# Performance work log

Measured on AMD Instinct MI355X. Metric: run time of the kernel, lower is better.

## Reference

```python
import jax, jax.numpy as jnp
import numpy as np

EPS = 1e-6      # vector-neuron epsilon
BN_EPS = 1e-5   # torch BatchNorm eps
NEG = 0.2       # LeakyReLU negative slope
K = 20


def knn_idx(flat, k):
    # flat: [B, D, N] flattened (C*3) features; returns kNN indices [B, N, k]
    xx = jnp.sum(flat * flat, axis=1)                     # [B, N]
    inner = jnp.einsum('bdn,bdm->bnm', flat, flat)        # [B, N, N]
    neg_dist = 2.0 * inner - xx[:, :, None] - xx[:, None, :]
    return jax.lax.top_k(neg_dist, k)[1]                  # [B, N, k]


def graph_feature(x, k):
    # x: [B, C, 3, N] -> [B, 2C, 3, N, k] = cat(neighbor - center, center)
    B, C, _, N = x.shape
    idx = knn_idx(x.reshape(B, C * 3, N), k)              # [B, N, k]
    xt = jnp.transpose(x, (0, 3, 1, 2))                   # [B, N, C, 3]
    nbr = jax.vmap(lambda f, i: f[i])(xt, idx)            # [B, N, k, C, 3]
    ctr = jnp.broadcast_to(xt[:, :, None], nbr.shape)
    feat = jnp.concatenate([nbr - ctr, ctr], axis=3)      # [B, N, k, 2C, 3]
    return jnp.transpose(feat, (0, 3, 4, 1, 2))


def vn_bn(x, w, b):
    # VNBatchNorm (training-mode batch stats): normalize the per-vector norm.
    # x: [B, C, 3, ...]
    norm = jnp.sqrt(jnp.sum(x * x, axis=2)) + EPS         # [B, C, ...]
    axes = (0,) + tuple(range(2, norm.ndim))
    mean = jnp.mean(norm, axis=axes, keepdims=True)
    var = jnp.mean((norm - mean) ** 2, axis=axes, keepdims=True)
    shp = (1, -1) + (1,) * (norm.ndim - 2)
    nbn = (norm - mean) / jnp.sqrt(var + BN_EPS) * w.reshape(shp) + b.reshape(shp)
    return x * jnp.expand_dims(nbn / norm, 2)


def vn_lrelu(x, wf, wd, bnw, bnb):
    # VNLinearLeakyReLU: linear over channel dim, VN batchnorm, directional LeakyReLU
    p = jnp.einsum('oi,bi...->bo...', wf, x)
    p = vn_bn(p, bnw, bnb)
    d = jnp.einsum('oi,bi...->bo...', wd, x)
    dot = jnp.sum(p * d, axis=2, keepdims=True)
    dsq = jnp.sum(d * d, axis=2, keepdims=True)
    mask = (dot >= 0).astype(x.dtype)
    return NEG * p + (1.0 - NEG) * (mask * p + (1.0 - mask) * (p - (dot / (dsq + EPS)) * d))


def setup_inputs() -> dict:
    key = jax.random.key(0)
    ks = jax.random.split(key, 12)
    H, C = 64, 128
    lin = lambda k, o, i: jax.random.normal(k, (o, i), jnp.float32) / np.sqrt(i)
    return {
        'x': jax.random.normal(ks[0], (8, 1024, 3), jnp.float32),
        'w1f': lin(ks[1], H, 2), 'w1d': lin(ks[2], H, 2),
        'bn1w': jnp.ones(H), 'bn1b': jnp.zeros(H),
        'w2f': lin(ks[3], H, 2 * H), 'w2d': lin(ks[4], H, 2 * H),
        'bn2w': jnp.ones(H), 'bn2b': jnp.zeros(H),
        'w3f': lin(ks[5], H, 2 * H), 'w3d': lin(ks[6], H, 2 * H),
        'bn3w': jnp.ones(H), 'bn3b': jnp.zeros(H),
        'w4f': lin(ks[7], H, 2 * H), 'w4d': lin(ks[8], H, 2 * H),
        'bn4w': jnp.ones(H), 'bn4b': jnp.zeros(H),
        'wcf': lin(ks[9], C, 4 * H), 'wcd': lin(ks[10], 1, 4 * H),
        'bncw': jnp.ones(C), 'bncb': jnp.zeros(C),
    }


def reference(x, w1f, w1d, bn1w, bn1b, w2f, w2d, bn2w, bn2b,
              w3f, w3d, bn3w, bn3b, w4f, w4d, bn4w, bn4b,
              wcf, wcd, bncw, bncb):
    pts = jnp.transpose(x, (0, 2, 1))[:, None]            # [B, 1, 3, N]
    h = vn_lrelu(graph_feature(pts, K), w1f, w1d, bn1w, bn1b)
    x1 = jnp.mean(h, axis=-1)                             # [B, H, 3, N]
    h = vn_lrelu(graph_feature(x1, K), w2f, w2d, bn2w, bn2b)
    x2 = jnp.mean(h, axis=-1)
    h = vn_lrelu(graph_feature(x2, K), w3f, w3d, bn3w, bn3b)
    x3 = jnp.mean(h, axis=-1)
    h = vn_lrelu(graph_feature(x3, K), w4f, w4d, bn4w, bn4b)
    x4 = jnp.mean(h, axis=-1)
    cat = jnp.concatenate([x1, x2, x3, x4], axis=1)       # [B, 4H, 3, N]
    out = vn_lrelu(cat, wcf, wcd, bncw, bncb)             # [B, c_dim, 3, N]
    return jnp.mean(out, axis=-1)                         # [B, c_dim, 3]
```

## Files before the change

kernel.cpp:

```cpp
#include <hip/hip_runtime.h>

#define NPTS 1024
#define NB 8
#define KNN 20
#define N3 (3*NPTS)
#define CHT 256
#define BSX (CHT*N3)

constexpr int OFF_X0    = 0;
constexpr int OFF_XFEAT = OFF_X0 + NB*N3;
constexpr int OFF_YAP   = OFF_XFEAT + NB*CHT*N3;
constexpr int OFF_YBP   = OFF_YAP + NB*N3*64;
constexpr int OFF_YAD   = OFF_YBP + NB*N3*64;
constexpr int OFF_YBD   = OFF_YAD + NB*N3*64;
constexpr int OFF_WCFT  = OFF_YBD + NB*N3*64;
constexpr int OFF_STATS = OFF_WCFT + 256*128;
constexpr int OFF_IDX   = OFF_STATS + 5*256;
constexpr int OFF_W4    = OFF_IDX + NB*NPTS*KNN;
constexpr int OFF_PF    = OFF_YAP;
constexpr int OFF_DF    = OFF_YAD;

__global__ __launch_bounds__(256) void k_prep(
    const float* __restrict__ x,
    const float* __restrict__ w1f, const float* __restrict__ w1d,
    const float* __restrict__ w2f, const float* __restrict__ w2d,
    const float* __restrict__ w3f, const float* __restrict__ w3d,
    const float* __restrict__ w4f, const float* __restrict__ w4d,
    const float* __restrict__ wcf,
    float* __restrict__ x0, float* __restrict__ w4, float* __restrict__ wT) {
  int blk = blockIdx.x, tid = threadIdx.x;
  if (blk < 32) {
    int t = blk*256 + tid;
    int b = t >> 10, n = t & 1023;
    const float* p = x + t*3;
    x0[b*N3 + n]          = p[0];
    x0[b*N3 + NPTS + n]   = p[1];
    x0[b*N3 + 2*NPTS + n] = p[2];
  } else if (blk == 32) {
    if (tid < 64) {
      int o = tid;
      float a0 = w1f[o*2], a1 = w1f[o*2+1];
      float d0 = w1d[o*2], d1 = w1d[o*2+1];
      float* dst = w4 + o*4;
      dst[0] = a0; dst[1] = a1 - a0; dst[2] = d0; dst[3] = d1 - d0;
    }
  } else if (blk < 36) {
    int L = blk - 32;
    const float* wf = (L == 1) ? w2f : (L == 2) ? w3f : w4f;
    const float* wd = (L == 1) ? w2d : (L == 2) ? w3d : w4d;
    float* dst = w4 + L*16384;
    for (int u = 0; u < 64; ++u) {
      int e = tid + u*256;
      int i = e >> 8, oc = e & 255, o = oc >> 2, c = oc & 3;
      float v;
      if (c == 0)      v = wf[o*128 + i];
      else if (c == 1) v = wf[o*128 + 64 + i] - wf[o*128 + i];
      else if (c == 2) v = wd[o*128 + i];
      else             v = wd[o*128 + 64 + i] - wd[o*128 + i];
      dst[e] = v;
    }
  } else {
    int e0 = (blk - 36) * 8192;
    for (int u = 0; u < 32; ++u) {
      int e = e0 + tid + u*256;
      int o = e >> 8, i = e & 255;
      wT[i*128 + o] = wcf[e];
    }
  }
}

__global__ __launch_bounds__(512) void k_knn3(const float* __restrict__ Fb, int bs, int D,
                                              int* __restrict__ idxo) {
  __shared__ float xs[2][8][NPTS];
  int g  = blockIdx.x;
  int wg = (g & 7)*32 + (g >> 3);
  int b  = wg >> 5;
  int n0 = (wg & 31) << 5;
  int tid = threadIdx.x;
  int w = tid >> 6, lane = tid & 63;
  int rowbase = n0 + (w << 2);
  const float* f = Fb + (size_t)b*bs;

  float acc[4][16], xxm[16], xxr[4];
  #pragma unroll
  for (int r = 0; r < 4; ++r) xxr[r] = 0.f;
  #pragma unroll
  for (int s = 0; s < 16; ++s) {
    xxm[s] = 0.f;
    #pragma unroll
    for (int r = 0; r < 4; ++r) acc[r][s] = 0.f;
  }

  int cnt0 = (D < 8) ? D : 8;
  #pragma unroll
  for (int u = 0; u < 4; ++u) {
    int e = tid + (u << 9);
    int dd = e >> 8, mq = (e & 255) << 2;
    if (dd < cnt0)
      *(float4*)&xs[0][dd][mq] = *(const float4*)&f[(size_t)dd*NPTS + mq];
  }
  __syncthreads();

  int nt = (D + 7) >> 3;
  for (int t = 0; t < nt; ++t) {
    int cur = t & 1;
    int cnt = D - (t << 3); if (cnt > 8) cnt = 8;
    float4 pf[4];
    if (t + 1 < nt) {
      int d0 = (t + 1) << 3;
      #pragma unroll
      for (int u = 0; u < 4; ++u) {
        int e = tid + (u << 9);
        int dd = e >> 8, mq = (e & 255) << 2;
        pf[u] = *(const float4*)&f[(size_t)(d0 + dd)*NPTS + mq];
      }
    }
    if (cnt == 8) {
      #pragma unroll
      for (int dd = 0; dd < 8; ++dd) {
        float4 rf = *(const float4*)&xs[cur][dd][rowbase];
        xxr[0] = fmaf(rf.x, rf.x, xxr[0]);
        xxr[1] = fmaf(rf.y, rf.y, xxr[1]);
        xxr[2] = fmaf(rf.z, rf.z, xxr[2]);
        xxr[3] = fmaf(rf.w, rf.w, xxr[3]);
        #pragma unroll
        for (int s2 = 0; s2 < 4; ++s2) {
          float4 xm = *(const float4*)&xs[cur][dd][(lane << 2) + (s2 << 8)];
          float xm4[4] = {xm.x, xm.y, xm.z, xm.w};
          #pragma unroll
          for (int q = 0; q < 4; ++q) {
            int s = s2*4 + q;
            xxm[s] = fmaf(xm4[q], xm4[q], xxm[s]);
            acc[0][s] = fmaf(rf.x, xm4[q], acc[0][s]);
            acc[1][s] = fmaf(rf.y, xm4[q], acc[1][s]);
            acc[2][s] = fmaf(rf.z, xm4[q], acc[2][s]);
            acc[3][s] = fmaf(rf.w, xm4[q], acc[3][s]);
          }
        }
      }
    } else {
      for (int dd = 0; dd < cnt; ++dd) {
        float4 rf = *(const float4*)&xs[cur][dd][rowbase];
        xxr[0] = fmaf(rf.x, rf.x, xxr[0]);
        xxr[1] = fmaf(rf.y, rf.y, xxr[1]);
        xxr[2] = fmaf(rf.z, rf.z, xxr[2]);
        xxr[3] = fmaf(rf.w, rf.w, xxr[3]);
        #pragma unroll
        for (int s2 = 0; s2 < 4; ++s2) {
          float4 xm = *(const float4*)&xs[cur][dd][(lane << 2) + (s2 << 8)];
          float xm4[4] = {xm.x, xm.y, xm.z, xm.w};
          #pragma unroll
          for (int q = 0; q < 4; ++q) {
            int s = s2*4 + q;
            xxm[s] = fmaf(xm4[q], xm4[q], xxm[s]);
            acc[0][s] = fmaf(rf.x, xm4[q], acc[0][s]);
            acc[1][s] = fmaf(rf.y, xm4[q], acc[1][s]);
            acc[2][s] = fmaf(rf.z, xm4[q], acc[2][s]);
            acc[3][s] = fmaf(rf.w, xm4[q], acc[3][s]);
          }
        }
      }
    }
    if (t + 1 < nt) {
      int nb = cur ^ 1;
      #pragma unroll
      for (int u = 0; u < 4; ++u) {
        int e = tid + (u << 9);
        int dd = e >> 8, mq = (e & 255) << 2;
        *(float4*)&xs[nb][dd][mq] = pf[u];
      }
    }
    __syncthreads();
  }

  #pragma unroll
  for (int r = 0; r < 4; ++r)
    #pragma unroll
    for (int s = 0; s < 16; ++s)
      acc[r][s] = (2.f*acc[r][s] - xxr[r]) - xxm[s];

  const float NEGINF = -3.402823466e38f;
  #pragma unroll
  for (int pr = 0; pr < 2; ++pr) {
    const int rA = pr*2, rB = pr*2 + 1;
    unsigned clA = 0xFFFFu, clB = 0xFFFFu;
    int winA = 0, winB = 0;
    for (int it = 0; it < KNN; ++it) {
      float boA = NEGINF, boB = NEGINF;
      unsigned bcA = 0u, bcB = 0u;
      #pragma unroll
      for (int s = 0; s < 16; ++s) {
        const unsigned Cs = (unsigned)(((s >> 2) << 8) | (s & 3));
        float vA = acc[rA][s]; vA = (clA == Cs) ? NEGINF : vA; acc[rA][s] = vA;
        if (vA > boA) { boA = vA; bcA = Cs; }
        float vB = acc[rB][s]; vB = (clB == Cs) ? NEGINF : vB; acc[rB][s] = vB;
        if (vB > boB) { boB = vB; bcB = Cs; }
      }
      int mA = (lane << 2) | (int)(bcA & 3u) | (int)(bcA & 0x300u);
      int mB = (lane << 2) | (int)(bcB & 3u) | (int)(bcB & 0x300u);
      float wmA = boA, wmB = boB;
      #pragma unroll
      for (int off = 1; off < 64; off <<= 1) {
        float tA = __shfl_xor(wmA, off, 64);
        float tB = __shfl_xor(wmB, off, 64);
        wmA = fmaxf(wmA, tA);
        wmB = fmaxf(wmB, tB);
      }
      unsigned long long balA = __ballot(boA == wmA);
      int win_mA;
      if (__popcll(balA) == 1) {
        int wl = __ffsll((long long)balA) - 1;
        win_mA = __shfl(mA, wl, 64);
      } else {
        int cA = (boA == wmA) ? (1023 - mA) : -1;
        #pragma unroll
        for (int off = 1; off < 64; off <<= 1) { int tc = __shfl_xor(cA, off, 64); cA = max(cA, tc); }
        win_mA = 1023 - cA;
      }
      clA = (boA == wmA && mA == win_mA) ? bcA : 0xFFFFu;
      if (lane == it) winA = win_mA;
      unsigned long long balB = __ballot(boB == wmB);
      int win_mB;
      if (__popcll(balB) == 1) {
        int wl = __ffsll((long long)balB) - 1;
        win_mB = __shfl(mB, wl, 64);
      } else {
        int cB = (boB == wmB) ? (1023 - mB) : -1;
        #pragma unroll
        for (int off = 1; off < 64; off <<= 1) { int tc = __shfl_xor(cB, off, 64); cB = max(cB, tc); }
        win_mB = 1023 - cB;
      }
      clB = (boB == wmB && mB == win_mB) ? bcB : 0xFFFFu;
      if (lane == it) winB = win_mB;
    }
    if (lane < KNN) {
      idxo[(b*NPTS + rowbase + rA)*KNN + lane] = winA;
      idxo[(b*NPTS + rowbase + rB)*KNN + lane] = winB;
    }
  }
}

__global__ __launch_bounds__(256) void k_linear4(const float* __restrict__ xin, int bsx,
                                                 const float* __restrict__ w4, int DIN,
                                                 float* __restrict__ yAp, float* __restrict__ yBp,
                                                 float* __restrict__ yAd, float* __restrict__ yBd) {
  int tid = threadIdx.x;
  int o = tid & 63, ns = tid >> 6;
  int b = blockIdx.y / 3, v = blockIdx.y % 3;
  int n0 = blockIdx.x * 32 + ns * 8;
  const float* xb = xin + (size_t)b*bsx + v*NPTS + n0;
  float aF[8], bF[8], aD[8], bD[8];
  #pragma unroll
  for (int j = 0; j < 8; ++j) { aF[j] = 0.f; bF[j] = 0.f; aD[j] = 0.f; bD[j] = 0.f; }
  #pragma unroll 4
  for (int i = 0; i < DIN; ++i) {
    float4 wv  = *(const float4*)&w4[(i << 8) + (o << 2)];
    float4 xlo = *(const float4*)&xb[i*N3];
    float4 xhi = *(const float4*)&xb[i*N3 + 4];
    float xv[8] = {xlo.x, xlo.y, xlo.z, xlo.w, xhi.x, xhi.y, xhi.z, xhi.w};
    #pragma unroll
    for (int j = 0; j < 8; ++j) {
      aF[j] = fmaf(wv.x, xv[j], aF[j]);
      bF[j] = fmaf(wv.y, xv[j], bF[j]);
      aD[j] = fmaf(wv.z, xv[j], aD[j]);
      bD[j] = fmaf(wv.w, xv[j], bD[j]);
    }
  }
  int base = ((b*3 + v)*NPTS + n0)*64 + o;
  #pragma unroll
  for (int j = 0; j < 8; ++j) {
    yAp[base + j*64] = aF[j];
    yBp[base + j*64] = bF[j];
    yAd[base + j*64] = aD[j];
    yBd[base + j*64] = bD[j];
  }
}

__global__ __launch_bounds__(256) void k_stats2(const float* __restrict__ yAp, const float* __restrict__ yBp,
                                                const int* __restrict__ idxo, float* __restrict__ statsL) {
  __shared__ float rs[256], rss[256];
  int tid = threadIdx.x; int o = tid & 63, w = tid >> 6;
  int blk = blockIdx.x;
  int wg = ((blk & 7) << 8) | (blk >> 3);
  int b = wg >> 8;
  int n = ((wg & 255) << 2) + w;
  const int* ir = idxo + (b*NPTS + n)*KNN;
  int4 ir0 = *(const int4*)&ir[0],  ir1 = *(const int4*)&ir[4];
  int4 ir2 = *(const int4*)&ir[8],  ir3 = *(const int4*)&ir[12];
  int4 ir4 = *(const int4*)&ir[16];
  int mm[20] = {ir0.x,ir0.y,ir0.z,ir0.w, ir1.x,ir1.y,ir1.z,ir1.w,
                ir2.x,ir2.y,ir2.z,ir2.w, ir3.x,ir3.y,ir3.z,ir3.w,
                ir4.x,ir4.y,ir4.z,ir4.w};
  int i0 = (b*3*NPTS + n)*64 + o;
  float c0 = yBp[i0], c1 = yBp[i0 + NPTS*64], c2 = yBp[i0 + 2*NPTS*64];
  float s = 0.f, ss = 0.f;
  #pragma unroll
  for (int kk = 0; kk < KNN; ++kk) {
    int m = mm[kk];
    int gg = (b*3*NPTS + m)*64 + o;
    float p0 = yAp[gg] + c0;
    float p1 = yAp[gg + NPTS*64] + c1;
    float p2 = yAp[gg + 2*NPTS*64] + c2;
    float nrm = sqrtf(p0*p0 + p1*p1 + p2*p2) + 1e-6f;
    s += nrm; ss = fmaf(nrm, nrm, ss);
  }
  rs[tid] = s; rss[tid] = ss;
  __syncthreads();
  if (tid < 64) {
    float a  = rs[tid]  + rs[tid+64]  + rs[tid+128]  + rs[tid+192];
    float as = rss[tid] + rss[tid+64] + rss[tid+128] + rss[tid+192];
    atomicAdd(&statsL[tid], a);
    atomicAdd(&statsL[128 + tid], as);
  }
}

__global__ __launch_bounds__(256) void k_apply(const float* __restrict__ yAp, const float* __restrict__ yBp,
                                               const float* __restrict__ yAd, const float* __restrict__ yBd,
                                               const int* __restrict__ idxo, const float* __restrict__ statsL,
                                               const float* __restrict__ bnw, const float* __restrict__ bnb,
                                               float* __restrict__ xfeat, int coff) {
  int tid = threadIdx.x; int o = tid & 63, w = tid >> 6;
  int blk = blockIdx.x;
  int wg = ((blk & 7) << 8) | (blk >> 3);
  int b = wg >> 8;
  int n = ((wg & 255) << 2) + w;
  const float cntInv = 1.f / 163840.f;
  float mean = statsL[o] * cntInv;
  float var  = statsL[128 + o] * cntInv - mean*mean;
  float istd = rsqrtf(var + 1e-5f);
  float wN = bnw[o], bN = bnb[o];
  int i0 = (b*3*NPTS + n)*64 + o;
  float cp0 = yBp[i0], cp1 = yBp[i0 + NPTS*64], cp2 = yBp[i0 + 2*NPTS*64];
  float cd0 = yBd[i0], cd1 = yBd[i0 + NPTS*64], cd2 = yBd[i0 + 2*NPTS*64];
  const int* ir = idxo + (b*NPTS + n)*KNN;
  int4 ir0 = *(const int4*)&ir[0],  ir1 = *(const int4*)&ir[4];
  int4 ir2 = *(const int4*)&ir[8],  ir3 = *(const int4*)&ir[12];
  int4 ir4 = *(const int4*)&ir[16];
  int mm[20] = {ir0.x,ir0.y,ir0.z,ir0.w, ir1.x,ir1.y,ir1.z,ir1.w,
                ir2.x,ir2.y,ir2.z,ir2.w, ir3.x,ir3.y,ir3.z,ir3.w,
                ir4.x,ir4.y,ir4.z,ir4.w};
  float a0 = 0.f, a1 = 0.f, a2 = 0.f;
  #pragma unroll
  for (int kk = 0; kk < KNN; ++kk) {
    int m = mm[kk];
    int gg = (b*3*NPTS + m)*64 + o;
    float p0 = yAp[gg] + cp0, p1 = yAp[gg + NPTS*64] + cp1, p2 = yAp[gg + 2*NPTS*64] + cp2;
    float d0 = yAd[gg] + cd0, d1 = yAd[gg + NPTS*64] + cd1, d2 = yAd[gg + 2*NPTS*64] + cd2;
    float nrm = sqrtf(p0*p0 + p1*p1 + p2*p2) + 1e-6f;
    float sc = ((nrm - mean)*istd*wN + bN) / nrm;
    p0 *= sc; p1 *= sc; p2 *= sc;
    float dot = p0*d0 + p1*d1 + p2*d2;
    float dsq = d0*d0 + d1*d1 + d2*d2;
    float coef = (dot < 0.f) ? (0.8f * dot / (dsq + 1e-6f)) : 0.f;
    a0 += p0 - coef*d0; a1 += p1 - coef*d1; a2 += p2 - coef*d2;
  }
  int ob = ((b*CHT + coff + o)*3)*NPTS + n;
  xfeat[ob]          = a0 * 0.05f;
  xfeat[ob + NPTS]   = a1 * 0.05f;
  xfeat[ob + 2*NPTS] = a2 * 0.05f;
}

__global__ __launch_bounds__(256) void k_pF3(const float* __restrict__ xfeat, const float* __restrict__ wT,
                                             const float* __restrict__ wcd,
                                             float* __restrict__ pF, float* __restrict__ dF) {
  __shared__ float xs[256][32];
  __shared__ float dpart[8][32];
  int tid = threadIdx.x;
  int b = blockIdx.y / 3, v = blockIdx.y % 3;
  int n0 = blockIdx.x * 32;
  const float* xb = xfeat + (size_t)b*BSX + v*NPTS + n0;
  #pragma unroll
  for (int u = 0; u < 8; ++u) {
    int e = tid + (u << 8);
    int i = e >> 3, sl = (e & 7) << 2;
    *(float4*)&xs[i][sl] = *(const float4*)&xb[i*N3 + sl];
  }
  __syncthreads();
  int o = tid & 127, h = tid >> 7;
  float a[16];
  #pragma unroll
  for (int j = 0; j < 16; ++j) a[j] = 0.f;
  for (int i = 0; i < 256; ++i) {
    float wv = wT[i*128 + o];
    #pragma unroll
    for (int q = 0; q < 4; ++q) {
      float4 xv = *(const float4*)&xs[i][h*16 + q*4];
      a[q*4+0] = fmaf(wv, xv.x, a[q*4+0]);
      a[q*4+1] = fmaf(wv, xv.y, a[q*4+1]);
      a[q*4+2] = fmaf(wv, xv.z, a[q*4+2]);
      a[q*4+3] = fmaf(wv, xv.w, a[q*4+3]);
    }
  }
  int base = ((b*3 + v)*NPTS + n0 + h*16)*128 + o;
  #pragma unroll
  for (int j = 0; j < 16; ++j) pF[base + j*128] = a[j];
  int nn = tid & 31, gI = tid >> 5;
  float dp = 0.f;
  for (int i = gI*32; i < gI*32 + 32; ++i) dp = fmaf(wcd[i], xs[i][nn], dp);
  dpart[gI][nn] = dp;
  __syncthreads();
  if (tid < 32) {
    float aa = 0.f;
    #pragma unroll
    for (int gq = 0; gq < 8; ++gq) aa += dpart[gq][tid];
    dF[(b*3 + v)*NPTS + n0 + tid] = aa;
  }
}

__global__ __launch_bounds__(256) void k_statsF2(const float* __restrict__ pF, float* __restrict__ statsF) {
  int tid = threadIdx.x; int o = tid & 127, half = tid >> 7;
  int blk = blockIdx.x;
  int b = blk >> 6, n0 = (blk & 63) << 4;
  float s = 0.f, ss = 0.f;
  for (int j = 0; j < 8; ++j) {
    int n = n0 + half + (j << 1);
    int g = (b*3*NPTS + n)*128 + o;
    float p0 = pF[g], p1 = pF[g + NPTS*128], p2 = pF[g + 2*NPTS*128];
    float nrm = sqrtf(p0*p0 + p1*p1 + p2*p2) + 1e-6f;
    s += nrm; ss = fmaf(nrm, nrm, ss);
  }
  atomicAdd(&statsF[o], s);
  atomicAdd(&statsF[128 + o], ss);
}

__global__ __launch_bounds__(256) void k_final2(const float* __restrict__ pF, const float* __restrict__ dF,
                                                const float* __restrict__ statsF,
                                                const float* __restrict__ bncw, const float* __restrict__ bncb,
                                                float* __restrict__ out) {
  int tid = threadIdx.x; int o = tid & 127, half = tid >> 7;
  int blk = blockIdx.x;
  int b = blk >> 5, n0 = (blk & 31) << 5;
  const float cntInv = 1.f / 8192.f;
  float mean = statsF[o] * cntInv;
  float var  = statsF[128 + o] * cntInv - mean*mean;
  float istd = rsqrtf(var + 1e-5f);
  float wN = bncw[o], bN = bncb[o];
  float a0 = 0.f, a1 = 0.f, a2 = 0.f;
  for (int j = 0; j < 16; ++j) {
    int n = n0 + half + (j << 1);
    int g = (b*3*NPTS + n)*128 + o;
    float p0 = pF[g], p1 = pF[g + NPTS*128], p2 = pF[g + 2*NPTS*128];
    int dg = b*N3 + n;
    float d0 = dF[dg], d1 = dF[dg + NPTS], d2 = dF[dg + 2*NPTS];
    float nrm = sqrtf(p0*p0 + p1*p1 + p2*p2) + 1e-6f;
    float sc = ((nrm - mean)*istd*wN + bN) / nrm;
    p0 *= sc; p1 *= sc; p2 *= sc;
    float dot = p0*d0 + p1*d1 + p2*d2;
    float dsq = d0*d0 + d1*d1 + d2*d2;
    float coef = (dot < 0.f) ? (0.8f * dot / (dsq + 1e-6f)) : 0.f;
    a0 += p0 - coef*d0; a1 += p1 - coef*d1; a2 += p2 - coef*d2;
  }
  float scl = 1.f / 1024.f;
  int ob = (b*128 + o)*3;
  atomicAdd(&out[ob],     a0*scl);
  atomicAdd(&out[ob + 1], a1*scl);
  atomicAdd(&out[ob + 2], a2*scl);
}

extern "C" void kernel_launch(void* const* d_in, const int* in_sizes, int n_in,
                              void* d_out, int out_size, void* d_ws, size_t ws_size,
                              hipStream_t stream) {
  (void)in_sizes; (void)n_in; (void)ws_size;
  const float* x = (const float*)d_in[0];
  const float* bnW[4] = {(const float*)d_in[3],  (const float*)d_in[7],
                         (const float*)d_in[11], (const float*)d_in[15]};
  const float* bnB[4] = {(const float*)d_in[4],  (const float*)d_in[8],
                         (const float*)d_in[12], (const float*)d_in[16]};
  const float* wcf  = (const float*)d_in[17];
  const float* wcd  = (const float*)d_in[18];
  const float* bncw = (const float*)d_in[19];
  const float* bncb = (const float*)d_in[20];

  float* ws    = (float*)d_ws;
  float* x0    = ws + OFF_X0;
  float* xfeat = ws + OFF_XFEAT;
  float* yAp   = ws + OFF_YAP;
  float* yBp   = ws + OFF_YBP;
  float* yAd   = ws + OFF_YAD;
  float* yBd   = ws + OFF_YBD;
  float* pF    = ws + OFF_PF;
  float* dF    = ws + OFF_DF;
  float* wT    = ws + OFF_WCFT;
  float* stats = ws + OFF_STATS;
  int*   idx   = (int*)(ws + OFF_IDX);
  float* w4    = ws + OFF_W4;

  hipMemsetAsync(stats, 0, 5*256*sizeof(float), stream);
  hipMemsetAsync(d_out, 0, (size_t)out_size*sizeof(float), stream);

  k_prep<<<40, 256, 0, stream>>>(x,
      (const float*)d_in[1], (const float*)d_in[2],
      (const float*)d_in[5], (const float*)d_in[6],
      (const float*)d_in[9], (const float*)d_in[10],
      (const float*)d_in[13], (const float*)d_in[14],
      wcf, x0, w4, wT);

  for (int L = 0; L < 4; ++L) {
    const float* fin = (L == 0) ? x0 : (xfeat + (L-1)*64*N3);
    int bs = (L == 0) ? N3 : BSX;
    int D  = (L == 0) ? 3 : 192;
    int DIN = (L == 0) ? 1 : 64;
    k_knn3<<<256, 512, 0, stream>>>(fin, bs, D, idx);
    k_linear4<<<dim3(32, 24), 256, 0, stream>>>(fin, bs, w4 + L*16384, DIN,
                                                yAp, yBp, yAd, yBd);
    k_stats2<<<2048, 256, 0, stream>>>(yAp, yBp, idx, stats + L*256);
    k_apply<<<2048, 256, 0, stream>>>(yAp, yBp, yAd, yBd, idx, stats + L*256,
                                      bnW[L], bnB[L], xfeat, L*64);
  }

  k_pF3<<<dim3(32, 24), 256, 0, stream>>>(xfeat, wT, wcd, pF, dF);
  k_statsF2<<<512, 256, 0, stream>>>(pF, stats + 4*256);
  k_final2<<<256, 256, 0, stream>>>(pF, dF, stats + 4*256, bncw, bncb, (float*)d_out);
}
```

Before: 1.034 ms.

## Split kNN into norm precompute and lighter two-row-per-wave kernel, finer pF tiles

Squared norms are now computed by a separate kernel instead of inside the kNN distance loop. The kNN kernel handles two rows per wave instead of four, over twice as many blocks, and keeps a single-buffered LDS tile with extra barriers. The aim is fewer registers, more occupancy and more parallelism in the serial top-k selection. The final projection kernel uses half-size point tiles for more blocks, and the memsets are folded into the prep kernel, at the cost of reloading the shared data tile once per row pair.

```diff
diff --git a/kernel.cpp b/kernel.cpp
--- a/kernel.cpp
+++ b/kernel.cpp
@@ -13,7 +13,8 @@
 constexpr int OFF_YBP   = OFF_YAP + NB*N3*64;
 constexpr int OFF_YAD   = OFF_YBP + NB*N3*64;
 constexpr int OFF_YBD   = OFF_YAD + NB*N3*64;
-constexpr int OFF_WCFT  = OFF_YBD + NB*N3*64;
+constexpr int OFF_XX    = OFF_YBD + NB*N3*64;
+constexpr int OFF_WCFT  = OFF_XX + NB*NPTS;
 constexpr int OFF_STATS = OFF_WCFT + 256*128;
 constexpr int OFF_IDX   = OFF_STATS + 5*256;
 constexpr int OFF_W4    = OFF_IDX + NB*NPTS*KNN;
@@ -27,7 +28,8 @@
     const float* __restrict__ w3f, const float* __restrict__ w3d,
     const float* __restrict__ w4f, const float* __restrict__ w4d,
     const float* __restrict__ wcf,
-    float* __restrict__ x0, float* __restrict__ w4, float* __restrict__ wT) {
+    float* __restrict__ x0, float* __restrict__ w4, float* __restrict__ wT,
+    float* __restrict__ stats, float* __restrict__ outz, int outn) {
   int blk = blockIdx.x, tid = threadIdx.x;
   if (blk < 32) {
     int t = blk*256 + tid;
@@ -59,54 +61,63 @@
       else             v = wd[o*128 + 64 + i] - wd[o*128 + i];
       dst[e] = v;
     }
-  } else {
+  } else if (blk < 40) {
     int e0 = (blk - 36) * 8192;
     for (int u = 0; u < 32; ++u) {
       int e = e0 + tid + u*256;
       int o = e >> 8, i = e & 255;
       wT[i*128 + o] = wcf[e];
     }
-  }
-}
-
-__global__ __launch_bounds__(512) void k_knn3(const float* __restrict__ Fb, int bs, int D,
+  } else {
+    for (int e = tid; e < 5*256; e += 256) stats[e] = 0.f;
+    for (int e = tid; e < outn; e += 256) outz[e] = 0.f;
+  }
+}
+
+__global__ void k_xx(const float* __restrict__ Fb, int bs, int D, float* __restrict__ xx) {
+  int t = blockIdx.x*256 + threadIdx.x;
+  int b = t >> 10, m = t & 1023;
+  const float* f = Fb + (size_t)b*bs + m;
+  float a = 0.f;
+  for (int d = 0; d < D; ++d) { float v = f[d*NPTS]; a = fmaf(v, v, a); }
+  xx[t] = a;
+}
+
+__global__ __launch_bounds__(512) void k_knn4(const float* __restrict__ Fb, int bs, int D,
+                                              const float* __restrict__ xx,
                                               int* __restrict__ idxo) {
-  __shared__ float xs[2][8][NPTS];
+  __shared__ float xs[8][NPTS];
   int g  = blockIdx.x;
-  int wg = (g & 7)*32 + (g >> 3);
-  int b  = wg >> 5;
-  int n0 = (wg & 31) << 5;
+  int wg = (g & 7)*64 + (g >> 3);
+  int b  = wg >> 6;
+  int n0 = (wg & 63) << 4;
   int tid = threadIdx.x;
   int w = tid >> 6, lane = tid & 63;
-  int rowbase = n0 + (w << 2);
+  int row0 = n0 + 2*w, row1 = row0 + 1;
   const float* f = Fb + (size_t)b*bs;
 
-  float acc[4][16], xxm[16], xxr[4];
-  #pragma unroll
-  for (int r = 0; r < 4; ++r) xxr[r] = 0.f;
-  #pragma unroll
-  for (int s = 0; s < 16; ++s) {
-    xxm[s] = 0.f;
+  float acc0[16], acc1[16];
+  #pragma unroll
+  for (int s = 0; s < 16; ++s) { acc0[s] = 0.f; acc1[s] = 0.f; }
+
+  int nt = (D + 7) >> 3;
+  {
+    int cnt = (D < 8) ? D : 8;
     #pragma unroll
-    for (int r = 0; r < 4; ++r) acc[r][s] = 0.f;
-  }
-
-  int cnt0 = (D < 8) ? D : 8;
-  #pragma unroll
-  for (int u = 0; u < 4; ++u) {
-    int e = tid + (u << 9);
-    int dd = e >> 8, mq = (e & 255) << 2;
-    if (dd < cnt0)
-      *(float4*)&xs[0][dd][mq] = *(const float4*)&f[(size_t)dd*NPTS + mq];
+    for (int u = 0; u < 4; ++u) {
+      int e = tid + (u << 9);
+      int dd = e >> 8, mq = (e & 255) << 2;
+      if (dd < cnt)
+        *(float4*)&xs[dd][mq] = *(const float4*)&f[(size_t)dd*NPTS + mq];
+    }
   }
   __syncthreads();
 
-  int nt = (D + 7) >> 3;
   for (int t = 0; t < nt; ++t) {
-    int cur = t & 1;
     int cnt = D - (t << 3); if (cnt > 8) cnt = 8;
     float4 pf[4];
-    if (t + 1 < nt) {
+    bool havenext = (t + 1 < nt);
+    if (havenext) {
       int d0 = (t + 1) << 3;
       #pragma unroll
       for (int u = 0; u < 4; ++u) {
@@ -118,125 +129,120 @@
     if (cnt == 8) {
       #pragma unroll
       for (int dd = 0; dd < 8; ++dd) {
-        float4 rf = *(const float4*)&xs[cur][dd][rowbase];
-        xxr[0] = fmaf(rf.x, rf.x, xxr[0]);
-        xxr[1] = fmaf(rf.y, rf.y, xxr[1]);
-        xxr[2] = fmaf(rf.z, rf.z, xxr[2]);
-        xxr[3] = fmaf(rf.w, rf.w, xxr[3]);
+        float rf0 = xs[dd][row0];
+        float rf1 = xs[dd][row1];
         #pragma unroll
         for (int s2 = 0; s2 < 4; ++s2) {
-          float4 xm = *(const float4*)&xs[cur][dd][(lane << 2) + (s2 << 8)];
-          float xm4[4] = {xm.x, xm.y, xm.z, xm.w};
-          #pragma unroll
-          for (int q = 0; q < 4; ++q) {
-            int s = s2*4 + q;
-            xxm[s] = fmaf(xm4[q], xm4[q], xxm[s]);
-            acc[0][s] = fmaf(rf.x, xm4[q], acc[0][s]);
-            acc[1][s] = fmaf(rf.y, xm4[q], acc[1][s]);
-            acc[2][s] = fmaf(rf.z, xm4[q], acc[2][s]);
-            acc[3][s] = fmaf(rf.w, xm4[q], acc[3][s]);
-          }
+          float4 xm = *(const float4*)&xs[dd][(lane << 2) + (s2 << 8)];
+          acc0[s2*4+0] = fmaf(rf0, xm.x, acc0[s2*4+0]);
+          acc0[s2*4+1] = fmaf(rf0, xm.y, acc0[s2*4+1]);
+          acc0[s2*4+2] = fmaf(rf0, xm.z, acc0[s2*4+2]);
+          acc0[s2*4+3] = fmaf(rf0, xm.w, acc0[s2*4+3]);
+          acc1[s2*4+0] = fmaf(rf1, xm.x, acc1[s2*4+0]);
+          acc1[s2*4+1] = fmaf(rf1, xm.y, acc1[s2*4+1]);
+          acc1[s2*4+2] = fmaf(rf1, xm.z, acc1[s2*4+2]);
+          acc1[s2*4+3] = fmaf(rf1, xm.w, acc1[s2*4+3]);
         }
       }
     } else {
       for (int dd = 0; dd < cnt; ++dd) {
-        float4 rf = *(const float4*)&xs[cur][dd][rowbase];
-        xxr[0] = fmaf(rf.x, rf.x, xxr[0]);
-        xxr[1] = fmaf(rf.y, rf.y, xxr[1]);
-        xxr[2] = fmaf(rf.z, rf.z, xxr[2]);
-        xxr[3] = fmaf(rf.w, rf.w, xxr[3]);
+        float rf0 = xs[dd][row0];
+        float rf1 = xs[dd][row1];
         #pragma unroll
         for (int s2 = 0; s2 < 4; ++s2) {
-          float4 xm = *(const float4*)&xs[cur][dd][(lane << 2) + (s2 << 8)];
-          float xm4[4] = {xm.x, xm.y, xm.z, xm.w};
-          #pragma unroll
-          for (int q = 0; q < 4; ++q) {
-            int s = s2*4 + q;
-            xxm[s] = fmaf(xm4[q], xm4[q], xxm[s]);
-            acc[0][s] = fmaf(rf.x, xm4[q], acc[0][s]);
-            acc[1][s] = fmaf(rf.y, xm4[q], acc[1][s]);
-            acc[2][s] = fmaf(rf.z, xm4[q], acc[2][s]);
-            acc[3][s] = fmaf(rf.w, xm4[q], acc[3][s]);
-          }
+          float4 xm = *(const float4*)&xs[dd][(lane << 2) + (s2 << 8)];
+          acc0[s2*4+0] = fmaf(rf0, xm.x, acc0[s2*4+0]);
+          acc0[s2*4+1] = fmaf(rf0, xm.y, acc0[s2*4+1]);
+          acc0[s2*4+2] = fmaf(rf0, xm.z, acc0[s2*4+2]);
+          acc0[s2*4+3] = fmaf(rf0, xm.w, acc0[s2*4+3]);
+          acc1[s2*4+0] = fmaf(rf1, xm.x, acc1[s2*4+0]);
+          acc1[s2*4+1] = fmaf(rf1, xm.y, acc1[s2*4+1]);
+          acc1[s2*4+2] = fmaf(rf1, xm.z, acc1[s2*4+2]);
+          acc1[s2*4+3] = fmaf(rf1, xm.w, acc1[s2*4+3]);
         }
       }
     }
-    if (t + 1 < nt) {
-      int nb = cur ^ 1;
+    if (havenext) {
+      __syncthreads();
       #pragma unroll
       for (int u = 0; u < 4; ++u) {
         int e = tid + (u << 9);
         int dd = e >> 8, mq = (e & 255) << 2;
-        *(float4*)&xs[nb][dd][mq] = pf[u];
+        *(float4*)&xs[dd][mq] = pf[u];
       }
-    }
-    __syncthreads();
-  }
-
-  #pragma unroll
-  for (int r = 0; r < 4; ++r)
+      __syncthreads();
+    }
+  }
+
+  float xxm[16];
+  #pragma unroll
+  for (int s2 = 0; s2 < 4; ++s2) {
+    float4 xv = *(const float4*)&xx[b*NPTS + (lane << 2) + (s2 << 8)];
+    xxm[s2*4+0] = xv.x; xxm[s2*4+1] = xv.y; xxm[s2*4+2] = xv.z; xxm[s2*4+3] = xv.w;
+  }
+  float xxr0 = xx[b*NPTS + row0];
+  float xxr1 = xx[b*NPTS + row1];
+  #pragma unroll
+  for (int s = 0; s < 16; ++s) {
+    acc0[s] = (2.f*acc0[s] - xxr0) - xxm[s];
+    acc1[s] = (2.f*acc1[s] - xxr1) - xxm[s];
+  }
+
+  const float NEGINF = -3.402823466e38f;
+  unsigned cl0 = 0xFFFFu, cl1 = 0xFFFFu;
+  int win0 = 0, win1 = 0;
+  for (int it = 0; it < KNN; ++it) {
+    float bo0 = NEGINF, bo1 = NEGINF;
+    unsigned bc0 = 0u, bc1 = 0u;
     #pragma unroll
-    for (int s = 0; s < 16; ++s)
-      acc[r][s] = (2.f*acc[r][s] - xxr[r]) - xxm[s];
-
-  const float NEGINF = -3.402823466e38f;
-  #pragma unroll
-  for (int pr = 0; pr < 2; ++pr) {
-    const int rA = pr*2, rB = pr*2 + 1;
-    unsigned clA = 0xFFFFu, clB = 0xFFFFu;
-    int winA = 0, winB = 0;
-    for (int it = 0; it < KNN; ++it) {
-      float boA = NEGINF, boB = NEGINF;
-      unsigned bcA = 0u, bcB = 0u;
+    for (int s = 0; s < 16; ++s) {
+      const unsigned Cs = (unsigned)(((s >> 2) << 8) | (s & 3));
+      float v0 = acc0[s]; v0 = (cl0 == Cs) ? NEGINF : v0; acc0[s] = v0;
+      if (v0 > bo0) { bo0 = v0; bc0 = Cs; }
+      float v1 = acc1[s]; v1 = (cl1 == Cs) ? NEGINF : v1; acc1[s] = v1;
+      if (v1 > bo1) { bo1 = v1; bc1 = Cs; }
+    }
+    int m0 = (lane << 2) | (int)(bc0 & 3u) | (int)(bc0 & 0x300u);
+    int m1 = (lane << 2) | (int)(bc1 & 3u) | (int)(bc1 & 0x300u);
+    float wm0 = bo0, wm1 = bo1;
+    #pragma unroll
+    for (int off = 1; off < 64; off <<= 1) {
+      float t0 = __shfl_xor(wm0, off, 64);
+      float t1 = __shfl_xor(wm1, off, 64);
+      wm0 = fmaxf(wm0, t0);
+      wm1 = fmaxf(wm1, t1);
+    }
+    unsigned long long bal0 = __ballot(bo0 == wm0);
+    int wmi0;
+    if (__popcll(bal0) == 1) {
+      int wl = __ffsll((long long)bal0) - 1;
+      wmi0 = __shfl(m0, wl, 64);
+    } else {
+      int c0 = (bo0 == wm0) ? (1023 - m0) : -1;
       #pragma unroll
-      for (int s = 0; s < 16; ++s) {
-        const unsigned Cs = (unsigned)(((s >> 2) << 8) | (s & 3));
-        float vA = acc[rA][s]; vA = (clA == Cs) ? NEGINF : vA; acc[rA][s] = vA;
-        if (vA > boA) { boA = vA; bcA = Cs; }
-        float vB = acc[rB][s]; vB = (clB == Cs) ? NEGINF : vB; acc[rB][s] = vB;
-        if (vB > boB) { boB = vB; bcB = Cs; }
-      }
-      int mA = (lane << 2) | (int)(bcA & 3u) | (int)(bcA & 0x300u);
-      int mB = (lane << 2) | (int)(bcB & 3u) | (int)(bcB & 0x300u);
-      float wmA = boA, wmB = boB;
+      for (int off = 1; off < 64; off <<= 1) { int tc = __shfl_xor(c0, off, 64); c0 = max(c0, tc); }
+      wmi0 = 1023 - c0;
+    }
+    cl0 = (bo0 == wm0 && m0 == wmi0) ? bc0 : 0xFFFFu;
+    if (lane == it) win0 = wmi0;
+
+    unsigned long long bal1 = __ballot(bo1 == wm1);
+    int wmi1;
+    if (__popcll(bal1) == 1) {
+      int wl = __ffsll((long long)bal1) - 1;
+      wmi1 = __shfl(m1, wl, 64);
+    } else {
+      int c1 = (bo1 == wm1) ? (1023 - m1) : -1;
       #pragma unroll
-      for (int off = 1; off < 64; off <<= 1) {
-        float tA = __shfl_xor(wmA, off, 64);
-        float tB = __shfl_xor(wmB, off, 64);
-        wmA = fmaxf(wmA, tA);
-        wmB = fmaxf(wmB, tB);
-      }
-      unsigned long long balA = __ballot(boA == wmA);
-      int win_mA;
-      if (__popcll(balA) == 1) {
-        int wl = __ffsll((long long)balA) - 1;
-        win_mA = __shfl(mA, wl, 64);
-      } else {
-        int cA = (boA == wmA) ? (1023 - mA) : -1;
-        #pragma unroll
-        for (int off = 1; off < 64; off <<= 1) { int tc = __shfl_xor(cA, off, 64); cA = max(cA, tc); }
-        win_mA = 1023 - cA;
-      }
-      clA = (boA == wmA && mA == win_mA) ? bcA : 0xFFFFu;
-      if (lane == it) winA = win_mA;
-      unsigned long long balB = __ballot(boB == wmB);
-      int win_mB;
-      if (__popcll(balB) == 1) {
-        int wl = __ffsll((long long)balB) - 1;
-        win_mB = __shfl(mB, wl, 64);
-      } else {
-        int cB = (boB == wmB) ? (1023 - mB) : -1;
-        #pragma unroll
-        for (int off = 1; off < 64; off <<= 1) { int tc = __shfl_xor(cB, off, 64); cB = max(cB, tc); }
-        win_mB = 1023 - cB;
-      }
-      clB = (boB == wmB && mB == win_mB) ? bcB : 0xFFFFu;
-      if (lane == it) winB = win_mB;
-    }
-    if (lane < KNN) {
-      idxo[(b*NPTS + rowbase + rA)*KNN + lane] = winA;
-      idxo[(b*NPTS + rowbase + rB)*KNN + lane] = winB;
-    }
+      for (int off = 1; off < 64; off <<= 1) { int tc = __shfl_xor(c1, off, 64); c1 = max(c1, tc); }
+      wmi1 = 1023 - c1;
+    }
+    cl1 = (bo1 == wm1 && m1 == wmi1) ? bc1 : 0xFFFFu;
+    if (lane == it) win1 = wmi1;
+  }
+  if (lane < KNN) {
+    idxo[(b*NPTS + row0)*KNN + lane] = win0;
+    idxo[(b*NPTS + row1)*KNN + lane] = win1;
   }
 }
 
@@ -360,49 +366,49 @@
   xfeat[ob + 2*NPTS] = a2 * 0.05f;
 }
 
-__global__ __launch_bounds__(256) void k_pF3(const float* __restrict__ xfeat, const float* __restrict__ wT,
+__global__ __launch_bounds__(256) void k_pF4(const float* __restrict__ xfeat, const float* __restrict__ wT,
                                              const float* __restrict__ wcd,
                                              float* __restrict__ pF, float* __restrict__ dF) {
-  __shared__ float xs[256][32];
-  __shared__ float dpart[8][32];
+  __shared__ float xs[256][16];
+  __shared__ float dpart[16][16];
   int tid = threadIdx.x;
   int b = blockIdx.y / 3, v = blockIdx.y % 3;
-  int n0 = blockIdx.x * 32;
+  int n0 = blockIdx.x * 16;
   const float* xb = xfeat + (size_t)b*BSX + v*NPTS + n0;
   #pragma unroll
-  for (int u = 0; u < 8; ++u) {
+  for (int u = 0; u < 4; ++u) {
     int e = tid + (u << 8);
-    int i = e >> 3, sl = (e & 7) << 2;
-    *(float4*)&xs[i][sl] = *(const float4*)&xb[i*N3 + sl];
+    int i = e >> 2, sl = (e & 3) << 2;
+    *(float4*)&xs[i][sl] = *(const float4*)&xb[(size_t)i*N3 + sl];
   }
   __syncthreads();
   int o = tid & 127, h = tid >> 7;
-  float a[16];
-  #pragma unroll
-  for (int j = 0; j < 16; ++j) a[j] = 0.f;
+  float a[8];
+  #pragma unroll
+  for (int j = 0; j < 8; ++j) a[j] = 0.f;
   for (int i = 0; i < 256; ++i) {
     float wv = wT[i*128 + o];
     #pragma unroll
-    for (int q = 0; q < 4; ++q) {
-      float4 xv = *(const float4*)&xs[i][h*16 + q*4];
+    for (int q = 0; q < 2; ++q) {
+      float4 xv = *(const float4*)&xs[i][h*8 + q*4];
       a[q*4+0] = fmaf(wv, xv.x, a[q*4+0]);
       a[q*4+1] = fmaf(wv, xv.y, a[q*4+1]);
       a[q*4+2] = fmaf(wv, xv.z, a[q*4+2]);
       a[q*4+3] = fmaf(wv, xv.w, a[q*4+3]);
     }
   }
-  int base = ((b*3 + v)*NPTS + n0 + h*16)*128 + o;
-  #pragma unroll
-  for (int j = 0; j < 16; ++j) pF[base + j*128] = a[j];
-  int nn = tid & 31, gI = tid >> 5;
+  int base = ((b*3 + v)*NPTS + n0 + h*8)*128 + o;
+  #pragma unroll
+  for (int j = 0; j < 8; ++j) pF[base + j*128] = a[j];
+  int nn = tid & 15, gI = tid >> 4;
   float dp = 0.f;
-  for (int i = gI*32; i < gI*32 + 32; ++i) dp = fmaf(wcd[i], xs[i][nn], dp);
+  for (int i = gI*16; i < gI*16 + 16; ++i) dp = fmaf(wcd[i], xs[i][nn], dp);
   dpart[gI][nn] = dp;
   __syncthreads();
-  if (tid < 32) {
+  if (tid < 16) {
     float aa = 0.f;
     #pragma unroll
-    for (int gq = 0; gq < 8; ++gq) aa += dpart[gq][tid];
+    for (int gq = 0; gq < 16; ++gq) aa += dpart[gq][tid];
     dF[(b*3 + v)*NPTS + n0 + tid] = aa;
   }
 }
@@ -480,27 +486,26 @@
   float* yBd   = ws + OFF_YBD;
   float* pF    = ws + OFF_PF;
   float* dF    = ws + OFF_DF;
+  float* xx    = ws + OFF_XX;
   float* wT    = ws + OFF_WCFT;
   float* stats = ws + OFF_STATS;
   int*   idx   = (int*)(ws + OFF_IDX);
   float* w4    = ws + OFF_W4;
 
-  hipMemsetAsync(stats, 0, 5*256*sizeof(float), stream);
-  hipMemsetAsync(d_out, 0, (size_t)out_size*sizeof(float), stream);
-
-  k_prep<<<40, 256, 0, stream>>>(x,
+  k_prep<<<41, 256, 0, stream>>>(x,
       (const float*)d_in[1], (const float*)d_in[2],
       (const float*)d_in[5], (const float*)d_in[6],
       (const float*)d_in[9], (const float*)d_in[10],
       (const float*)d_in[13], (const float*)d_in[14],
-      wcf, x0, w4, wT);
+      wcf, x0, w4, wT, stats, (float*)d_out, out_size);
 
   for (int L = 0; L < 4; ++L) {
     const float* fin = (L == 0) ? x0 : (xfeat + (L-1)*64*N3);
     int bs = (L == 0) ? N3 : BSX;
     int D  = (L == 0) ? 3 : 192;
     int DIN = (L == 0) ? 1 : 64;
-    k_knn3<<<256, 512, 0, stream>>>(fin, bs, D, idx);
+    k_xx<<<NB*NPTS/256, 256, 0, stream>>>(fin, bs, D, xx);
+    k_knn4<<<512, 512, 0, stream>>>(fin, bs, D, xx, idx);
     k_linear4<<<dim3(32, 24), 256, 0, stream>>>(fin, bs, w4 + L*16384, DIN,
                                                 yAp, yBp, yAd, yBd);
     k_stats2<<<2048, 256, 0, stream>>>(yAp, yBp, idx, stats + L*256);
@@ -508,7 +513,7 @@
                                       bnW[L], bnB[L], xfeat, L*64);
   }
 
-  k_pF3<<<dim3(32, 24), 256, 0, stream>>>(xfeat, wT, wcd, pF, dF);
+  k_pF4<<<dim3(64, 24), 256, 0, stream>>>(xfeat, wT, wcd, pF, dF);
   k_statsF2<<<512, 256, 0, stream>>>(pF, stats + 4*256);
   k_final2<<<256, 256, 0, stream>>>(pF, dF, stats + 4*256, bncw, bncb, (float*)d_out);
 }
```

Result: slower. 1.217 ms (+17.7%).
